# Kernel optimization log

Hardware: AMD Instinct MI355X
Metric: run time of the kernel (lower is better)

Reference implementation:

```python
import jax, jax.numpy as jnp
import numpy as np

N_NODES = 100000
N_EDGES = 3200000
IN_DIM = 128
HID_DIM = 64
OUT_DIM = 2
N_GRAPHS = 512


def setup_inputs() -> dict:
    key = jax.random.key(0)
    ks = jax.random.split(key, 8)
    x = jax.random.normal(ks[0], (N_NODES, IN_DIM), dtype=jnp.float32)
    edge_index = jax.random.randint(ks[1], (2, N_EDGES), 0, N_NODES, dtype=jnp.int64)
    batch = jnp.sort(jax.random.randint(ks[2], (N_NODES,), 0, N_GRAPHS, dtype=jnp.int64))
    # GCNConv params (glorot-ish scale)
    W_gcn = jax.random.normal(ks[3], (IN_DIM, HID_DIM), dtype=jnp.float32) / np.sqrt(IN_DIM)
    b_gcn = jnp.zeros((HID_DIM,), dtype=jnp.float32)
    # MLP params: Linear(hid,hid) -> ReLU -> Linear(hid,out)
    W1 = jax.random.normal(ks[4], (HID_DIM, HID_DIM), dtype=jnp.float32) / np.sqrt(HID_DIM)
    b1 = jnp.zeros((HID_DIM,), dtype=jnp.float32)
    W2 = jax.random.normal(ks[5], (HID_DIM, OUT_DIM), dtype=jnp.float32) / np.sqrt(HID_DIM)
    b2 = jnp.zeros((OUT_DIM,), dtype=jnp.float32)
    return {"x": x, "edge_index": edge_index, "batch": batch,
            "W_gcn": W_gcn, "b_gcn": b_gcn, "W1": W1, "b1": b1, "W2": W2, "b2": b2}


def reference(x, edge_index, batch, W_gcn, b_gcn, W1, b1, W2, b2):
    n = x.shape[0]
    # --- GCNConv: add self-loops, symmetric normalization, aggregate, transform ---
    self_loop = jnp.arange(n, dtype=edge_index.dtype)
    row = jnp.concatenate([edge_index[0], self_loop])  # source nodes
    col = jnp.concatenate([edge_index[1], self_loop])  # target nodes
    deg = jax.ops.segment_sum(jnp.ones_like(col, dtype=x.dtype), col, num_segments=n)
    dinv = jnp.where(deg > 0, jax.lax.rsqrt(deg), 0.0)
    norm = dinv[row] * dinv[col]                       # (E+N,)
    xw = x @ W_gcn                                     # (N, hid) transform first (in_dim > hid)
    msg = xw[row] * norm[:, None]                      # gather + scale
    z = jax.ops.segment_sum(msg, col, num_segments=n) + b_gcn  # scatter-add
    z = jax.nn.relu(z)
    # --- global mean pool over graphs ---
    sums = jax.ops.segment_sum(z, batch, num_segments=N_GRAPHS)          # (G, hid)
    cnts = jax.ops.segment_sum(jnp.ones((n,), z.dtype), batch, num_segments=N_GRAPHS)
    g = sums / jnp.maximum(cnts, 1.0)[:, None]
    # --- MLP -> sigmoid ---
    h = jax.nn.relu(g @ W1 + b1)
    return jax.nn.sigmoid(h @ W2 + b2)                 # (G, out_dim)
```

## Files before the change

### kernel.cpp

```cpp
#include <hip/hip_runtime.h>

#define N_NODES 100000
#define N_EDGES 3200000
#define IN_DIM 128
#define HID_DIM 64
#define OUT_DIM 2
#define N_GRAPHS 512

#define BSHIFT 6
#define NBUCK 1564
#define NB3 256
#define EPB 12500
#define NSB 391
#define LDS_E2 3072
#define ZERO_ROW N_NODES

__device__ inline int xcol(int b) { return ((b & 7) << 5) | (b >> 3); }

__device__ inline float uaf(unsigned int u) {
    union { unsigned int i; float f; } v; v.i = u; return v.f;
}
__device__ inline unsigned short f2bf(float f) {
    union { float f; unsigned int i; } v; v.f = f;
    unsigned int r = v.i + 0x7fffu + ((v.i >> 16) & 1u);
    return (unsigned short)(r >> 16);
}

typedef __attribute__((ext_vector_type(8))) short bf16x8;
typedef __attribute__((ext_vector_type(4))) float f32x4;
typedef __attribute__((ext_vector_type(2))) float f32x2;

__global__ __launch_bounds__(512) void k_hist(const int* __restrict__ col,
                                              int* __restrict__ H) {
    __shared__ int h[NBUCK];
    for (int i = threadIdx.x; i < NBUCK; i += 512) h[i] = 0;
    __syncthreads();
    int b = blockIdx.x;
    int bb = xcol(b);
    int s = b * EPB, e = s + EPB;
    for (int i = s + threadIdx.x; i < e; i += 512)
        atomicAdd(&h[col[i] >> BSHIFT], 1);
    __syncthreads();
    for (int i = threadIdx.x; i < NBUCK; i += 512)
        H[i * NB3 + bb] = h[i];
}

__global__ __launch_bounds__(1024) void k_scan_a(const int* __restrict__ H,
                                                 int* __restrict__ OFF,
                                                 int* __restrict__ bsum) {
    __shared__ int lds[1024];
    int i = blockIdx.x * 1024 + threadIdx.x;
    int v = H[i];
    lds[threadIdx.x] = v;
    __syncthreads();
    for (int off = 1; off < 1024; off <<= 1) {
        int t = (threadIdx.x >= off) ? lds[threadIdx.x - off] : 0;
        __syncthreads();
        lds[threadIdx.x] += t;
        __syncthreads();
    }
    OFF[i] = lds[threadIdx.x] - v;
    if (threadIdx.x == 1023) bsum[blockIdx.x] = lds[1023];
}

__global__ __launch_bounds__(1024) void k_scan_b(int* __restrict__ OFF,
                                                 const int* __restrict__ bsum,
                                                 float* __restrict__ gsum,
                                                 float* __restrict__ gcnt,
                                                 unsigned char* __restrict__ xws) {
    __shared__ int ls[NSB];
    for (int i = threadIdx.x; i < NSB; i += 1024) ls[i] = bsum[i];
    __syncthreads();
    if (threadIdx.x == 0) {
        int run = 0;
        for (int b = 0; b < NSB; b++) { int t = ls[b]; ls[b] = run; run += t; }
    }
    __syncthreads();
    int i = blockIdx.x * 1024 + threadIdx.x;
    OFF[i] += ls[blockIdx.x];
    if (blockIdx.x < 32) gsum[blockIdx.x * 1024 + threadIdx.x] = 0.f;
    if (blockIdx.x == 33 && threadIdx.x < N_GRAPHS) gcnt[threadIdx.x] = 0.f;
    if (blockIdx.x == 32 && threadIdx.x < 16)
        ((int*)(xws + (size_t)ZERO_ROW * HID_DIM))[threadIdx.x] = 0;
}

__global__ __launch_bounds__(512) void k_scatter(const int* __restrict__ row,
                                                 const int* __restrict__ col,
                                                 const int* __restrict__ OFF,
                                                 int* __restrict__ binned) {
    __shared__ int lofs[NBUCK];
    __shared__ int cur[NBUCK];
    int b = blockIdx.x;
    int bb = xcol(b);
    for (int i = threadIdx.x; i < NBUCK; i += 512) {
        lofs[i] = OFF[i * NB3 + bb];
        cur[i] = 0;
    }
    __syncthreads();
    int s = b * EPB, e = s + EPB;
    for (int i = s + threadIdx.x; i < e; i += 512) {
        int c = col[i];
        int r = row[i];
        int bk = c >> BSHIFT;
        int rk = atomicAdd(&cur[bk], 1);
        binned[lofs[bk] + rk] = ((c & 63) << 17) | r;
    }
}

__global__ __launch_bounds__(256) void k_deg(const int* __restrict__ binned,
                                             const int* __restrict__ OFF,
                                             int* __restrict__ degs,
                                             float* __restrict__ dinv) {
    int bkt = blockIdx.x;
    int s = OFF[bkt * NB3];
    int e = (bkt == NBUCK - 1) ? N_EDGES : OFF[(bkt + 1) * NB3];
    __shared__ int cnt[64];
    if (threadIdx.x < 64) cnt[threadIdx.x] = 0;
    __syncthreads();
    for (int i = s + threadIdx.x; i < e; i += 256)
        atomicAdd(&cnt[binned[i] >> 17], 1);
    __syncthreads();
    int n = (bkt << BSHIFT) + threadIdx.x;
    if (threadIdx.x < 64 && n < N_NODES) {
        degs[n] = cnt[threadIdx.x];
        dinv[n] = rsqrtf((float)cnt[threadIdx.x] + 1.0f);
    }
}

__global__ __launch_bounds__(256) void k_gemm(const float* __restrict__ x,
                                              const float* __restrict__ Wg,
                                              const float* __restrict__ dinv,
                                              unsigned char* __restrict__ xws) {
    __shared__ unsigned short wb[16][64][8];

    for (int idx = threadIdx.x; idx < 1024; idx += 256) {
        int f = idx >> 6, l = idx & 63;
        int ks = f >> 2, nt = f & 3;
        int n = (l & 15) + (nt << 4);
        int kbase = (ks << 5) + ((l >> 4) << 3);
        unsigned short tmp[8];
#pragma unroll
        for (int j = 0; j < 8; j++)
            tmp[j] = f2bf(Wg[(kbase + j) * HID_DIM + n]);
        *(bf16x8*)&wb[f][l][0] = *(const bf16x8*)tmp;
    }
    __syncthreads();

    int wave = threadIdx.x >> 6;
    int lane = threadIdx.x & 63;
    int q = lane >> 4, nn = lane & 15;

    bf16x8 bfrag[4][4];
#pragma unroll
    for (int ks = 0; ks < 4; ks++)
#pragma unroll
        for (int nt = 0; nt < 4; nt++)
            bfrag[ks][nt] = *(const bf16x8*)&wb[ks * 4 + nt][lane][0];

    int node0 = blockIdx.x * 64 + wave * 16;
    int arow = node0 + nn;
    if (arow > N_NODES - 1) arow = N_NODES - 1;
    const float* xrow = x + (size_t)arow * IN_DIM + (q << 3);

    f32x4 acc[4] = {{0.f,0.f,0.f,0.f},{0.f,0.f,0.f,0.f},
                    {0.f,0.f,0.f,0.f},{0.f,0.f,0.f,0.f}};
#pragma unroll
    for (int ks = 0; ks < 4; ks++) {
        float4 xa = *(const float4*)(xrow + ks * 32);
        float4 xb_ = *(const float4*)(xrow + ks * 32 + 4);
        bf16x8 af;
        af[0] = (short)f2bf(xa.x); af[1] = (short)f2bf(xa.y);
        af[2] = (short)f2bf(xa.z); af[3] = (short)f2bf(xa.w);
        af[4] = (short)f2bf(xb_.x); af[5] = (short)f2bf(xb_.y);
        af[6] = (short)f2bf(xb_.z); af[7] = (short)f2bf(xb_.w);
#pragma unroll
        for (int nt = 0; nt < 4; nt++)
            acc[nt] = __builtin_amdgcn_mfma_f32_16x16x32_bf16(af, bfrag[ks][nt], acc[nt], 0, 0, 0);
    }

#pragma unroll
    for (int r = 0; r < 4; r++) {
        int mrow = node0 + q * 4 + r;
        if (mrow < N_NODES) {
            float dn = dinv[mrow];
            int p01 = __builtin_amdgcn_cvt_pk_fp8_f32(acc[0][r] * dn, acc[1][r] * dn, 0, false);
            int p23 = __builtin_amdgcn_cvt_pk_fp8_f32(acc[2][r] * dn, acc[3][r] * dn, 0, false);
            unsigned char* rp = xws + (size_t)mrow * HID_DIM + nn;
            rp[0]  = (unsigned char)(p01 & 0xff);
            rp[16] = (unsigned char)((p01 >> 8) & 0xff);
            rp[32] = (unsigned char)(p23 & 0xff);
            rp[48] = (unsigned char)((p23 >> 8) & 0xff);
        }
    }
}

__global__ __launch_bounds__(256) void k_aggrf(const unsigned char* __restrict__ xws,
                                               const int* __restrict__ binned,
                                               const int* __restrict__ OFF,
                                               const int* __restrict__ degs,
                                               const int* __restrict__ batch,
                                               const float* __restrict__ bg,
                                               float* __restrict__ gsum,
                                               float* __restrict__ gcnt) {
    int bkt = blockIdx.x;
    int nbase = bkt << BSHIFT;
    if (nbase >= N_NODES) return;
    int nnodes = N_NODES - nbase; if (nnodes > 64) nnodes = 64;
    int s = OFF[bkt * NB3];
    int e = (bkt == NBUCK - 1) ? N_EDGES : OFF[(bkt + 1) * NB3];
    int m = e - s;

    __shared__ int cnt[64];
    __shared__ int lptr[65];
    __shared__ int cur[64];
    __shared__ int sb[64];
    __shared__ float gcl[8];
    __shared__ alignas(16) int srt[LDS_E2];
    __shared__ float pool[4][4][64];

    if (threadIdx.x < 64) {
        int n = nbase + threadIdx.x;
        cnt[threadIdx.x] = (threadIdx.x < nnodes) ? degs[n] : 0;
        sb[threadIdx.x]  = (threadIdx.x < nnodes) ? batch[n] : 0;
        cur[threadIdx.x] = 0;
    }
    if (threadIdx.x < 8) gcl[threadIdx.x] = 0.f;
    for (int t = threadIdx.x; t < 4 * 4 * 64; t += 256)
        ((float*)pool)[t] = 0.f;
    __syncthreads();

    if (threadIdx.x < 64) {
        int v = (cnt[threadIdx.x] + 16) & ~15;
        int run = v;
#pragma unroll
        for (int off = 1; off < 64; off <<= 1) {
            int t = __shfl_up(run, off);
            if (threadIdx.x >= off) run += t;
        }
        lptr[threadIdx.x + 1] = run;
        if (threadIdx.x == 0) lptr[0] = 0;
    }
    __syncthreads();
    int tot = lptr[64]; if (tot > LDS_E2) tot = LDS_E2;
    for (int i = threadIdx.x; i < tot; i += 256) srt[i] = ZERO_ROW << 6;
    __syncthreads();
    if (threadIdx.x < nnodes) {
        int p = lptr[threadIdx.x] + cnt[threadIdx.x];
        if (p < LDS_E2) srt[p] = (nbase + threadIdx.x) << 6;
        int sl = sb[threadIdx.x] - sb[0];
        if (sl < 8) atomicAdd(&gcl[sl], 1.0f);
        else atomicAdd(&gcnt[sb[threadIdx.x]], 1.0f);
    }
    for (int i = threadIdx.x; i < m; i += 256) {
        int pk = binned[s + i];
        int nid = pk >> 17;
        int rk = atomicAdd(&cur[nid], 1);
        int pos = lptr[nid] + rk;
        if (pos < LDS_E2) srt[pos] = (pk & 0x1FFFF) << 6;
    }
    __syncthreads();

    int wave = threadIdx.x >> 6;
    int lane = threadIdx.x & 63;
    int sub = lane >> 3;
    int lc  = lane & 7;
    int l8  = lc << 3;
    const unsigned char* xbl = xws + l8;
    int g0 = sb[0];
    float4 bia0, bia1;
    { const float4* bgv = (const float4*)bg;
      bia0 = bgv[lc * 2]; bia1 = bgv[lc * 2 + 1]; }

    for (int k = 0; k < 16; k++) {
        int ln = wave * 16 + k;
        if (ln >= nnodes) break;
        int s0 = lptr[ln], e0 = lptr[ln + 1];
        if (s0 > LDS_E2) s0 = LDS_E2;
        if (e0 > LDS_E2) e0 = LDS_E2;
        f32x2 a0 = {0.f,0.f}, a1 = {0.f,0.f}, a2 = {0.f,0.f}, a3 = {0.f,0.f};
        for (int i = s0; i < e0; i += 16) {
            int2 rr = *(const int2*)&srt[i + (sub << 1)];
            uint2 q0 = *(const uint2*)(xbl + rr.x);
            uint2 q1 = *(const uint2*)(xbl + rr.y);
            f32x2 p;
            p = __builtin_amdgcn_cvt_pk_f32_fp8(q0.x, false); a0 += p;
            p = __builtin_amdgcn_cvt_pk_f32_fp8(q0.x, true);  a1 += p;
            p = __builtin_amdgcn_cvt_pk_f32_fp8(q0.y, false); a2 += p;
            p = __builtin_amdgcn_cvt_pk_f32_fp8(q0.y, true);  a3 += p;
            p = __builtin_amdgcn_cvt_pk_f32_fp8(q1.x, false); a0 += p;
            p = __builtin_amdgcn_cvt_pk_f32_fp8(q1.x, true);  a1 += p;
            p = __builtin_amdgcn_cvt_pk_f32_fp8(q1.y, false); a2 += p;
            p = __builtin_amdgcn_cvt_pk_f32_fp8(q1.y, true);  a3 += p;
        }
        float r0 = a0[0], r1 = a0[1], r2 = a1[0], r3 = a1[1];
        float r4 = a2[0], r5 = a2[1], r6 = a3[0], r7 = a3[1];
#define RED8(x) x += __shfl_xor(x, 8); x += __shfl_xor(x, 16); x += __shfl_xor(x, 32);
        RED8(r0) RED8(r1) RED8(r2) RED8(r3) RED8(r4) RED8(r5) RED8(r6) RED8(r7)
#undef RED8
        if (sub == 0) {
            float dn = rsqrtf((float)cnt[ln] + 1.0f);
            float4 v0, v1;
            v0.x = fmaxf(r0 * dn + bia0.x, 0.f);
            v0.y = fmaxf(r1 * dn + bia0.y, 0.f);
            v0.z = fmaxf(r2 * dn + bia0.z, 0.f);
            v0.w = fmaxf(r3 * dn + bia0.w, 0.f);
            v1.x = fmaxf(r4 * dn + bia1.x, 0.f);
            v1.y = fmaxf(r5 * dn + bia1.y, 0.f);
            v1.z = fmaxf(r6 * dn + bia1.z, 0.f);
            v1.w = fmaxf(r7 * dn + bia1.w, 0.f);
            int slot = sb[ln] - g0;
            if (slot < 4) {
                float4* pp = (float4*)&pool[wave][slot][l8];
                float4 p0 = pp[0], p1 = pp[1];
                p0.x += v0.x; p0.y += v0.y; p0.z += v0.z; p0.w += v0.w;
                p1.x += v1.x; p1.y += v1.y; p1.z += v1.z; p1.w += v1.w;
                pp[0] = p0; pp[1] = p1;
            } else {
                float* gp = &gsum[sb[ln] * HID_DIM + l8];
                atomicAdd(gp + 0, v0.x); atomicAdd(gp + 1, v0.y);
                atomicAdd(gp + 2, v0.z); atomicAdd(gp + 3, v0.w);
                atomicAdd(gp + 4, v1.x); atomicAdd(gp + 5, v1.y);
                atomicAdd(gp + 6, v1.z); atomicAdd(gp + 7, v1.w);
            }
        }
    }
    __syncthreads();

    if (threadIdx.x < 8) {
        float c = gcl[threadIdx.x];
        if (c != 0.f) atomicAdd(&gcnt[g0 + threadIdx.x], c);
    }
    for (int t = threadIdx.x; t < 4 * 64; t += 256) {
        int slot = t >> 6, j = t & 63;
        float v = pool[0][slot][j] + pool[1][slot][j]
                + pool[2][slot][j] + pool[3][slot][j];
        if (v != 0.f) atomicAdd(&gsum[(g0 + slot) * HID_DIM + j], v);
    }
}

__global__ __launch_bounds__(64) void k_mlp(const float* __restrict__ gsum,
                                            const float* __restrict__ gcnt,
                                            const float* __restrict__ W1,
                                            const float* __restrict__ b1,
                                            const float* __restrict__ W2,
                                            const float* __restrict__ b2,
                                            float* __restrict__ out) {
    int g = blockIdx.x;
    int j = threadIdx.x;
    float cnt = fmaxf(gcnt[g], 1.0f);

    __shared__ float gs[64];
    __shared__ float hs[64];
    gs[j] = gsum[g * 64 + j] / cnt;
    __syncthreads();

    float h = b1[j];
    for (int k = 0; k < 64; k++) h += gs[k] * W1[k * 64 + j];
    hs[j] = fmaxf(h, 0.f);
    __syncthreads();

    if (j < OUT_DIM) {
        float o = b2[j];
        for (int k = 0; k < 64; k++) o += hs[k] * W2[k * OUT_DIM + j];
        out[g * OUT_DIM + j] = 1.f / (1.f + expf(-o));
    }
}

extern "C" void kernel_launch(void* const* d_in, const int* in_sizes, int n_in,
                              void* d_out, int out_size, void* d_ws, size_t ws_size,
                              hipStream_t stream) {
    const float* x   = (const float*)d_in[0];
    const int* eidx  = (const int*)d_in[1];
    const int* batch = (const int*)d_in[2];
    const float* Wg  = (const float*)d_in[3];
    const float* bg  = (const float*)d_in[4];
    const float* W1  = (const float*)d_in[5];
    const float* b1  = (const float*)d_in[6];
    const float* W2  = (const float*)d_in[7];
    const float* b2  = (const float*)d_in[8];
    float* out = (float*)d_out;

    char* w = (char*)d_ws;
    unsigned char* xws = (unsigned char*)w;     w += (size_t)(N_NODES + 1) * HID_DIM;
    int*   binned  = (int*)w;                   w += (size_t)N_EDGES * 4;
    int*   H       = (int*)w;                   w += (size_t)NBUCK * NB3 * 4;
    int*   OFF     = (int*)w;                   w += (size_t)NBUCK * NB3 * 4;
    int*   bsum    = (int*)w;                   w += NSB * 4;
    int*   degs    = (int*)w;                   w += N_NODES * 4;
    float* dinv    = (float*)w;                 w += N_NODES * 4;
    float* gsum    = (float*)w;                 w += N_GRAPHS * HID_DIM * 4;
    float* gcnt    = (float*)w;                 w += N_GRAPHS * 4;

    const int* rowp = eidx;
    const int* colp = eidx + N_EDGES;

    k_hist<<<NB3, 512, 0, stream>>>(colp, H);
    k_scan_a<<<NSB, 1024, 0, stream>>>(H, OFF, bsum);
    k_scan_b<<<NSB, 1024, 0, stream>>>(OFF, bsum, gsum, gcnt, xws);
    k_scatter<<<NB3, 512, 0, stream>>>(rowp, colp, OFF, binned);
    k_deg<<<NBUCK, 256, 0, stream>>>(binned, OFF, degs, dinv);
    k_gemm<<<(N_NODES + 63) / 64, 256, 0, stream>>>(x, Wg, dinv, xws);
    k_aggrf<<<NBUCK, 256, 0, stream>>>(xws, binned, OFF, degs, batch, bg, gsum, gcnt);
    k_mlp<<<N_GRAPHS, 64, 0, stream>>>(gsum, gcnt, W1, b1, W2, b2, out);
}
```

Baseline: 221.4 us.

## Restructure aggregation to 16 lanes per node, 4 nodes per wave, 512 threads

The aggregation kernel now runs 512 threads per bucket. Each wave processes 4 nodes at a time, with 16 lanes per node each owning 4 feature bytes. The old layout had 8 lanes per feature slice plus a cross-lane shuffle reduction. The new one removes the shuffle reductions and cuts per-node padding from multiples of 16 to multiples of 4, which reduces wasted zero-row gathers for low-degree nodes. The trade-offs are fewer parallel edge gathers per node (lanes walk the edge list sequentially), possible load imbalance between nodes sharing a wave, and a smaller LDS edge buffer.

```diff
diff --git a/kernel.cpp b/kernel.cpp
--- a/kernel.cpp
+++ b/kernel.cpp
@@ -12,7 +12,7 @@
 #define NB3 256
 #define EPB 12500
 #define NSB 391
-#define LDS_E2 3072
+#define LDS_E2 2816
 #define ZERO_ROW N_NODES
 
 __device__ inline int xcol(int b) { return ((b & 7) << 5) | (b >> 3); }
@@ -194,7 +194,7 @@
     }
 }
 
-__global__ __launch_bounds__(256) void k_aggrf(const unsigned char* __restrict__ xws,
+__global__ __launch_bounds__(512) void k_aggrf(const unsigned char* __restrict__ xws,
                                                const int* __restrict__ binned,
                                                const int* __restrict__ OFF,
                                                const int* __restrict__ degs,
@@ -216,7 +216,7 @@
     __shared__ int sb[64];
     __shared__ float gcl[8];
     __shared__ alignas(16) int srt[LDS_E2];
-    __shared__ float pool[4][4][64];
+    __shared__ float pool[8][4][64];
 
     if (threadIdx.x < 64) {
         int n = nbase + threadIdx.x;
@@ -225,12 +225,12 @@
         cur[threadIdx.x] = 0;
     }
     if (threadIdx.x < 8) gcl[threadIdx.x] = 0.f;
-    for (int t = threadIdx.x; t < 4 * 4 * 64; t += 256)
+    for (int t = threadIdx.x; t < 8 * 4 * 64; t += 512)
         ((float*)pool)[t] = 0.f;
     __syncthreads();
 
     if (threadIdx.x < 64) {
-        int v = (cnt[threadIdx.x] + 16) & ~15;
+        int v = (threadIdx.x < nnodes) ? ((cnt[threadIdx.x] + 4) & ~3) : 0;
         int run = v;
 #pragma unroll
         for (int off = 1; off < 64; off <<= 1) {
@@ -242,7 +242,7 @@
     }
     __syncthreads();
     int tot = lptr[64]; if (tot > LDS_E2) tot = LDS_E2;
-    for (int i = threadIdx.x; i < tot; i += 256) srt[i] = ZERO_ROW << 6;
+    for (int i = threadIdx.x; i < tot; i += 512) srt[i] = ZERO_ROW << 6;
     __syncthreads();
     if (threadIdx.x < nnodes) {
         int p = lptr[threadIdx.x] + cnt[threadIdx.x];
@@ -251,7 +251,7 @@
         if (sl < 8) atomicAdd(&gcl[sl], 1.0f);
         else atomicAdd(&gcnt[sb[threadIdx.x]], 1.0f);
     }
-    for (int i = threadIdx.x; i < m; i += 256) {
+    for (int i = threadIdx.x; i < m; i += 512) {
         int pk = binned[s + i];
         int nid = pk >> 17;
         int rk = atomicAdd(&cur[nid], 1);
@@ -262,66 +262,61 @@
 
     int wave = threadIdx.x >> 6;
     int lane = threadIdx.x & 63;
-    int sub = lane >> 3;
-    int lc  = lane & 7;
-    int l8  = lc << 3;
-    const unsigned char* xbl = xws + l8;
+    int sub = lane >> 4;
+    int lc  = lane & 15;
+    int l4  = lc << 2;
+    const unsigned char* xbl = xws + l4;
     int g0 = sb[0];
-    float4 bia0, bia1;
-    { const float4* bgv = (const float4*)bg;
-      bia0 = bgv[lc * 2]; bia1 = bgv[lc * 2 + 1]; }
-
-    for (int k = 0; k < 16; k++) {
-        int ln = wave * 16 + k;
-        if (ln >= nnodes) break;
-        int s0 = lptr[ln], e0 = lptr[ln + 1];
+    float4 bia = ((const float4*)bg)[lc];
+
+#pragma unroll
+    for (int r = 0; r < 2; r++) {
+        int ln = wave * 8 + sub * 2 + r;
+        int valid = (ln < nnodes);
+        int s0 = valid ? lptr[ln] : 0;
+        int e0 = valid ? lptr[ln + 1] : 0;
         if (s0 > LDS_E2) s0 = LDS_E2;
         if (e0 > LDS_E2) e0 = LDS_E2;
-        f32x2 a0 = {0.f,0.f}, a1 = {0.f,0.f}, a2 = {0.f,0.f}, a3 = {0.f,0.f};
-        for (int i = s0; i < e0; i += 16) {
-            int2 rr = *(const int2*)&srt[i + (sub << 1)];
-            uint2 q0 = *(const uint2*)(xbl + rr.x);
-            uint2 q1 = *(const uint2*)(xbl + rr.y);
+        f32x2 alo = {0.f, 0.f}, ahi = {0.f, 0.f};
+        for (int i = s0; i < e0; i += 4) {
+            int4 rr = *(const int4*)&srt[i];
+            unsigned int d0 = *(const unsigned int*)(xbl + rr.x);
+            unsigned int d1 = *(const unsigned int*)(xbl + rr.y);
+            unsigned int d2 = *(const unsigned int*)(xbl + rr.z);
+            unsigned int d3 = *(const unsigned int*)(xbl + rr.w);
             f32x2 p;
-            p = __builtin_amdgcn_cvt_pk_f32_fp8(q0.x, false); a0 += p;
-            p = __builtin_amdgcn_cvt_pk_f32_fp8(q0.x, true);  a1 += p;
-            p = __builtin_amdgcn_cvt_pk_f32_fp8(q0.y, false); a2 += p;
-            p = __builtin_amdgcn_cvt_pk_f32_fp8(q0.y, true);  a3 += p;
-            p = __builtin_amdgcn_cvt_pk_f32_fp8(q1.x, false); a0 += p;
-            p = __builtin_amdgcn_cvt_pk_f32_fp8(q1.x, true);  a1 += p;
-            p = __builtin_amdgcn_cvt_pk_f32_fp8(q1.y, false); a2 += p;
-            p = __builtin_amdgcn_cvt_pk_f32_fp8(q1.y, true);  a3 += p;
-        }
-        float r0 = a0[0], r1 = a0[1], r2 = a1[0], r3 = a1[1];
-        float r4 = a2[0], r5 = a2[1], r6 = a3[0], r7 = a3[1];
-#define RED8(x) x += __shfl_xor(x, 8); x += __shfl_xor(x, 16); x += __shfl_xor(x, 32);
-        RED8(r0) RED8(r1) RED8(r2) RED8(r3) RED8(r4) RED8(r5) RED8(r6) RED8(r7)
-#undef RED8
-        if (sub == 0) {
+            p = __builtin_amdgcn_cvt_pk_f32_fp8(d0, false); alo += p;
+            p = __builtin_amdgcn_cvt_pk_f32_fp8(d0, true);  ahi += p;
+            p = __builtin_amdgcn_cvt_pk_f32_fp8(d1, false); alo += p;
+            p = __builtin_amdgcn_cvt_pk_f32_fp8(d1, true);  ahi += p;
+            p = __builtin_amdgcn_cvt_pk_f32_fp8(d2, false); alo += p;
+            p = __builtin_amdgcn_cvt_pk_f32_fp8(d2, true);  ahi += p;
+            p = __builtin_amdgcn_cvt_pk_f32_fp8(d3, false); alo += p;
+            p = __builtin_amdgcn_cvt_pk_f32_fp8(d3, true);  ahi += p;
+        }
+        int slot = 99;
+        float4 val;
+        if (valid) {
             float dn = rsqrtf((float)cnt[ln] + 1.0f);
-            float4 v0, v1;
-            v0.x = fmaxf(r0 * dn + bia0.x, 0.f);
-            v0.y = fmaxf(r1 * dn + bia0.y, 0.f);
-            v0.z = fmaxf(r2 * dn + bia0.z, 0.f);
-            v0.w = fmaxf(r3 * dn + bia0.w, 0.f);
-            v1.x = fmaxf(r4 * dn + bia1.x, 0.f);
-            v1.y = fmaxf(r5 * dn + bia1.y, 0.f);
-            v1.z = fmaxf(r6 * dn + bia1.z, 0.f);
-            v1.w = fmaxf(r7 * dn + bia1.w, 0.f);
-            int slot = sb[ln] - g0;
-            if (slot < 4) {
-                float4* pp = (float4*)&pool[wave][slot][l8];
-                float4 p0 = pp[0], p1 = pp[1];
-                p0.x += v0.x; p0.y += v0.y; p0.z += v0.z; p0.w += v0.w;
-                p1.x += v1.x; p1.y += v1.y; p1.z += v1.z; p1.w += v1.w;
-                pp[0] = p0; pp[1] = p1;
-            } else {
-                float* gp = &gsum[sb[ln] * HID_DIM + l8];
-                atomicAdd(gp + 0, v0.x); atomicAdd(gp + 1, v0.y);
-                atomicAdd(gp + 2, v0.z); atomicAdd(gp + 3, v0.w);
-                atomicAdd(gp + 4, v1.x); atomicAdd(gp + 5, v1.y);
-                atomicAdd(gp + 6, v1.z); atomicAdd(gp + 7, v1.w);
+            val.x = fmaxf(alo[0] * dn + bia.x, 0.f);
+            val.y = fmaxf(alo[1] * dn + bia.y, 0.f);
+            val.z = fmaxf(ahi[0] * dn + bia.z, 0.f);
+            val.w = fmaxf(ahi[1] * dn + bia.w, 0.f);
+            slot = sb[ln] - g0;
+        }
+#pragma unroll
+        for (int ss = 0; ss < 4; ss++) {
+            if (sub == ss && slot < 4) {
+                float4* pp = (float4*)&pool[wave][slot][l4];
+                float4 pv = *pp;
+                pv.x += val.x; pv.y += val.y; pv.z += val.z; pv.w += val.w;
+                *pp = pv;
             }
+        }
+        if (slot >= 4 && slot < 99) {
+            float* gp = &gsum[sb[ln] * HID_DIM + l4];
+            atomicAdd(gp + 0, val.x); atomicAdd(gp + 1, val.y);
+            atomicAdd(gp + 2, val.z); atomicAdd(gp + 3, val.w);
         }
     }
     __syncthreads();
@@ -330,10 +325,11 @@
         float c = gcl[threadIdx.x];
         if (c != 0.f) atomicAdd(&gcnt[g0 + threadIdx.x], c);
     }
-    for (int t = threadIdx.x; t < 4 * 64; t += 256) {
+    for (int t = threadIdx.x; t < 4 * 64; t += 512) {
         int slot = t >> 6, j = t & 63;
-        float v = pool[0][slot][j] + pool[1][slot][j]
-                + pool[2][slot][j] + pool[3][slot][j];
+        float v = 0.f;
+#pragma unroll
+        for (int w2 = 0; w2 < 8; w2++) v += pool[w2][slot][j];
         if (v != 0.f) atomicAdd(&gsum[(g0 + slot) * HID_DIM + j], v);
     }
 }
@@ -400,6 +396,6 @@
     k_scatter<<<NB3, 512, 0, stream>>>(rowp, colp, OFF, binned);
     k_deg<<<NBUCK, 256, 0, stream>>>(binned, OFF, degs, dinv);
     k_gemm<<<(N_NODES + 63) / 64, 256, 0, stream>>>(x, Wg, dinv, xws);
-    k_aggrf<<<NBUCK, 256, 0, stream>>>(xws, binned, OFF, degs, batch, bg, gsum, gcnt);
+    k_aggrf<<<NBUCK, 512, 0, stream>>>(xws, binned, OFF, degs, batch, bg, gsum, gcnt);
     k_mlp<<<N_GRAPHS, 64, 0, stream>>>(gsum, gcnt, W1, b1, W2, b2, out);
 }
```

Result: faster. 203.7 us (-8.0%).
